# Performance work log

Hardware: AMD Instinct MI355X
Metric: run time of the kernel (lower is better)

Reference implementation:

```python
import jax, jax.numpy as jnp
import numpy as np

N = 50000

def _norm_coeffs(edge_index, n):
    # add self-loops, compute symmetric GCN normalization D^-1/2 (A+I) D^-1/2
    loops = jnp.arange(n, dtype=edge_index.dtype)
    src = jnp.concatenate([edge_index[0], loops])
    dst = jnp.concatenate([edge_index[1], loops])
    deg = jax.ops.segment_sum(jnp.ones_like(dst, dtype=jnp.float32), dst, num_segments=n)
    dinv = jnp.where(deg > 0, jax.lax.rsqrt(deg), 0.0)
    norm = dinv[src] * dinv[dst]  # [E+N]
    return src, dst, norm

def _gcn(x, W, b, src, dst, norm, n):
    h = x @ W                                   # [N, out]
    m = h[src] * norm[:, None]                  # [E+N, out] gather + scale
    return jax.ops.segment_sum(m, dst, num_segments=n) + b

def setup_inputs() -> dict:
    key = jax.random.key(0)
    ks = jax.random.split(key, 8)
    d, h = 96, 96
    E = 800000
    return {
        "x": jax.random.normal(ks[0], (N, d), jnp.float32),
        "edge_index": jax.random.randint(ks[1], (2, E), 0, N, dtype=jnp.int64),
        "h_prev": jax.random.normal(ks[2], (N, h), jnp.float32),
        "Wx": jax.random.normal(ks[3], (d, h), jnp.float32) * (1.0 / np.sqrt(d)),
        "bx": jnp.zeros((h,), jnp.float32),
        "Wuh": jax.random.normal(ks[4], (2 * h, h), jnp.float32) * (1.0 / np.sqrt(2 * h)),
        "buh": jnp.zeros((h,), jnp.float32),
        "Wch": jax.random.normal(ks[5], (2 * h, h), jnp.float32) * (1.0 / np.sqrt(2 * h)),
        "bch": jnp.zeros((h,), jnp.float32),
    }

def reference(x, edge_index, h_prev, Wx, bx, Wuh, buh, Wch, bch):
    n = x.shape[0]
    src, dst, norm = _norm_coeffs(edge_index, n)
    x_gcn = _gcn(x, Wx, bx, src, dst, norm, n)
    combined = jnp.concatenate([x_gcn, h_prev], axis=1)
    # original computes gcn_uh(combined) twice for u and r; identical math -> compute once
    g = jax.nn.sigmoid(_gcn(combined, Wuh, buh, src, dst, norm, n))
    u = g
    r = g
    combined_r = jnp.concatenate([x_gcn, r * h_prev], axis=1)
    c = jnp.tanh(_gcn(combined_r, Wch, bch, src, dst, norm, n))
    return u * h_prev + (1.0 - u) * c
```

## Files before the change

kernel.cpp:

```cpp
#include <hip/hip_runtime.h>
#include <hip/hip_bf16.h>

#define D 96
#define CAP 64
typedef long long i64;

typedef __bf16 bf16x8 __attribute__((ext_vector_type(8)));
typedef float f32x16 __attribute__((ext_vector_type(16)));

__device__ __forceinline__ float bf2f(unsigned short u) {
  union { unsigned u; float f; } x; x.u = ((unsigned)u) << 16; return x.f;
}
__device__ __forceinline__ void unpack8(uint4 p, float* a) {
  a[0] = bf2f((unsigned short)(p.x & 0xffff)); a[1] = bf2f((unsigned short)(p.x >> 16));
  a[2] = bf2f((unsigned short)(p.y & 0xffff)); a[3] = bf2f((unsigned short)(p.y >> 16));
  a[4] = bf2f((unsigned short)(p.z & 0xffff)); a[5] = bf2f((unsigned short)(p.z >> 16));
  a[6] = bf2f((unsigned short)(p.w & 0xffff)); a[7] = bf2f((unsigned short)(p.w >> 16));
}

__global__ __launch_bounds__(256) void k_detect(const unsigned* __restrict__ w,
                                                int* flag, int E) {
  if (threadIdx.x < 64) {
    int lane = threadIdx.x;
    int lim = (E < 2048) ? E : 2048;
    unsigned acc = 0;
    for (int j = lane; j < lim; j += 64) acc |= w[2 * j + 1];
#pragma unroll
    for (int off = 32; off > 0; off >>= 1) acc |= __shfl_down(acc, off, 64);
    if (lane == 0) *flag = (acc == 0) ? 1 : 0;
  }
}

__global__ __launch_bounds__(256) void k_bucket(const int* __restrict__ e32,
                                                const i64* __restrict__ e64,
                                                const int* __restrict__ flagp,
                                                uint2* __restrict__ region,
                                                int* __restrict__ cntmat,
                                                int E, int N, int NB) {
  __shared__ int lofs[256];
  const int tid = threadIdx.x;
  const int blk = blockIdx.x;
  lofs[tid] = 0;
  __syncthreads();
  const int f = *flagp;
  const int chunk = (E + gridDim.x - 1) / gridDim.x;
  const int lo = blk * chunk;
  const int hi = min(E, lo + chunk);
  for (int i = lo + tid; i < hi; i += 256) {
    int d, s;
    if (f) { d = (int)e64[(size_t)E + i]; s = (int)e64[i]; }
    else   { d = e32[(size_t)E + i];      s = e32[i]; }
    if ((unsigned)d >= (unsigned)N || (unsigned)s >= (unsigned)N) continue;
    int q = d >> 8;
    int r = atomicAdd(&lofs[q], 1);
    if (r < CAP)
      region[((size_t)q * 256 + blk) * CAP + r] = make_uint2((unsigned)s, (unsigned)d);
  }
  __syncthreads();
  if (tid < NB) cntmat[blk * 256 + tid] = min(lofs[tid], CAP);
}

__global__ __launch_bounds__(256) void k_csr(const uint2* __restrict__ region,
                                             const int* __restrict__ cntmat,
                                             int* __restrict__ deg,
                                             int* __restrict__ csrp, int NB) {
  __shared__ int ldeg[256];
  __shared__ int lcsr[256 * CAP];
  const int tid = threadIdx.x;
  const int b = blockIdx.x;
  ldeg[tid] = 0;
  __syncthreads();
  int cnt = cntmat[tid * 256 + b];
  const uint2* cell = region + ((size_t)b * 256 + tid) * CAP;
  for (int k = 0; k < cnt; k++) {
    uint2 e = cell[k];
    int node = (int)(e.y & 255u);
    int r = atomicAdd(&ldeg[node], 1);
    if (r < CAP) lcsr[node * CAP + r] = (int)e.x;
  }
  __syncthreads();
  deg[(b << 8) + tid] = ldeg[tid];
  const uint4* src = (const uint4*)lcsr;
  uint4* dst = (uint4*)(csrp + ((size_t)b << 8) * CAP);
#pragma unroll
  for (int it = 0; it < (256 * CAP) / 4 / 256; it++)
    dst[tid + it * 256] = src[tid + it * 256];
}

template <int KTOT, int MODE>
__global__ __launch_bounds__(256) void gemm_mfma(
    const float* __restrict__ xin, const float* __restrict__ xg,
    const float* __restrict__ hprev, const float* __restrict__ gmul,
    const float* __restrict__ W, const int* __restrict__ deg,
    __hip_bfloat16* __restrict__ t, int N) {
  __shared__ __align__(16) unsigned short Ah[4][129][8];
  __shared__ __align__(16) unsigned short Al[4][129][8];
  __shared__ __align__(16) unsigned short Wh[4][97][8];
  __shared__ __align__(16) unsigned short Wl[4][97][8];
  const int tid = threadIdx.x;
  const int lane = tid & 63;
  const int wave = tid >> 6;
  const int lr = lane & 31;
  const int kg = lane >> 5;
  const int rb = blockIdx.x * 128;

  f32x16 acc0, acc1, acc2;
#pragma unroll
  for (int i = 0; i < 16; i++) { acc0[i] = 0.f; acc1[i] = 0.f; acc2[i] = 0.f; }

  const int arow = tid >> 3;
  const int ak0 = (tid & 7) * 4;

  for (int kc = 0; kc < KTOT; kc += 32) {
    if (kc) __syncthreads();
#pragma unroll
    for (int p = 0; p < 4; p++) {
      int row = arow + p * 32;
      int grow = rb + row;
      float4 v = make_float4(0.f, 0.f, 0.f, 0.f);
      int gk = kc + ak0;
      if (grow < N) {
        if (MODE == 0) {
          v = *(const float4*)&xin[(size_t)grow * D + gk];
        } else if (gk < 96) {
          v = *(const float4*)&xg[(size_t)grow * D + gk];
        } else {
          v = *(const float4*)&hprev[(size_t)grow * D + (gk - 96)];
          if (MODE == 2) {
            float4 gm = *(const float4*)&gmul[(size_t)grow * D + (gk - 96)];
            v.x *= gm.x; v.y *= gm.y; v.z *= gm.z; v.w *= gm.w;
          }
        }
      }
      unsigned ux = __float_as_uint(v.x), uy = __float_as_uint(v.y);
      unsigned uz = __float_as_uint(v.z), uw = __float_as_uint(v.w);
      unsigned h01 = (uy & 0xffff0000u) | (ux >> 16);
      unsigned h23 = (uw & 0xffff0000u) | (uz >> 16);
      float lx = v.x - __uint_as_float(ux & 0xffff0000u);
      float ly = v.y - __uint_as_float(uy & 0xffff0000u);
      float lz = v.z - __uint_as_float(uz & 0xffff0000u);
      float lw = v.w - __uint_as_float(uw & 0xffff0000u);
      unsigned l01 = (__float_as_uint(ly) & 0xffff0000u) | (__float_as_uint(lx) >> 16);
      unsigned l23 = (__float_as_uint(lw) & 0xffff0000u) | (__float_as_uint(lz) >> 16);
      int kb = ak0 >> 3, ki = ak0 & 7;
      *(uint2*)&Ah[kb][row][ki] = make_uint2(h01, h23);
      *(uint2*)&Al[kb][row][ki] = make_uint2(l01, l23);
    }
#pragma unroll
    for (int p = 0; p < 3; p++) {
      int idx = tid + p * 256;
      int kq = idx / 96;
      int c = idx - kq * 96;
      int k0 = kq * 4;
      const float* wp = &W[(size_t)(kc + k0) * D + c];
      float w0 = wp[0], w1 = wp[D], w2 = wp[2 * D], w3 = wp[3 * D];
      unsigned u0 = __float_as_uint(w0), u1 = __float_as_uint(w1);
      unsigned u2 = __float_as_uint(w2), u3 = __float_as_uint(w3);
      unsigned h01 = (u1 & 0xffff0000u) | (u0 >> 16);
      unsigned h23 = (u3 & 0xffff0000u) | (u2 >> 16);
      float l0 = w0 - __uint_as_float(u0 & 0xffff0000u);
      float l1 = w1 - __uint_as_float(u1 & 0xffff0000u);
      float l2 = w2 - __uint_as_float(u2 & 0xffff0000u);
      float l3 = w3 - __uint_as_float(u3 & 0xffff0000u);
      unsigned l01 = (__float_as_uint(l1) & 0xffff0000u) | (__float_as_uint(l0) >> 16);
      unsigned l23 = (__float_as_uint(l3) & 0xffff0000u) | (__float_as_uint(l2) >> 16);
      int kb = k0 >> 3, ki = k0 & 7;
      *(uint2*)&Wh[kb][c][ki] = make_uint2(h01, h23);
      *(uint2*)&Wl[kb][c][ki] = make_uint2(l01, l23);
    }
    __syncthreads();
#pragma unroll
    for (int s = 0; s < 2; s++) {
      int kb = 2 * s + kg;
      bf16x8 ah = *(const bf16x8*)&Ah[kb][32 * wave + lr][0];
      bf16x8 al = *(const bf16x8*)&Al[kb][32 * wave + lr][0];
      bf16x8 b0h = *(const bf16x8*)&Wh[kb][lr][0];
      bf16x8 b1h = *(const bf16x8*)&Wh[kb][32 + lr][0];
      bf16x8 b2h = *(const bf16x8*)&Wh[kb][64 + lr][0];
      bf16x8 b0l = *(const bf16x8*)&Wl[kb][lr][0];
      bf16x8 b1l = *(const bf16x8*)&Wl[kb][32 + lr][0];
      bf16x8 b2l = *(const bf16x8*)&Wl[kb][64 + lr][0];
      acc0 = __builtin_amdgcn_mfma_f32_32x32x16_bf16(ah, b0h, acc0, 0, 0, 0);
      acc1 = __builtin_amdgcn_mfma_f32_32x32x16_bf16(ah, b1h, acc1, 0, 0, 0);
      acc2 = __builtin_amdgcn_mfma_f32_32x32x16_bf16(ah, b2h, acc2, 0, 0, 0);
      acc0 = __builtin_amdgcn_mfma_f32_32x32x16_bf16(al, b0h, acc0, 0, 0, 0);
      acc1 = __builtin_amdgcn_mfma_f32_32x32x16_bf16(al, b1h, acc1, 0, 0, 0);
      acc2 = __builtin_amdgcn_mfma_f32_32x32x16_bf16(al, b2h, acc2, 0, 0, 0);
      acc0 = __builtin_amdgcn_mfma_f32_32x32x16_bf16(ah, b0l, acc0, 0, 0, 0);
      acc1 = __builtin_amdgcn_mfma_f32_32x32x16_bf16(ah, b1l, acc1, 0, 0, 0);
      acc2 = __builtin_amdgcn_mfma_f32_32x32x16_bf16(ah, b2l, acc2, 0, 0, 0);
    }
  }
  const int rbase = rb + 32 * wave + 4 * kg;
#pragma unroll
  for (int r = 0; r < 16; r++) {
    int row = rbase + (r & 3) + 8 * (r >> 2);
    if (row >= N) continue;
    float dv = rsqrtf((float)deg[row] + 1.0f);
    __hip_bfloat16* tp = &t[(size_t)row * D];
    tp[lr]      = __float2bfloat16(acc0[r] * dv);
    tp[lr + 32] = __float2bfloat16(acc1[r] * dv);
    tp[lr + 64] = __float2bfloat16(acc2[r] * dv);
  }
}

template <int MODE>
__global__ __launch_bounds__(256) void gather_fin(
    const __hip_bfloat16* __restrict__ t, const int* __restrict__ deg,
    const int* __restrict__ csrp,
    const float* __restrict__ bias,
    const float* __restrict__ g, const float* __restrict__ hprev,
    float* __restrict__ outf, int N) {
  int idx = blockIdx.x * 256 + threadIdx.x;
  int total = N * 12;
  if (idx >= total) return;
  int v = idx / 12;
  int c8 = idx - v * 12;
  const uint4* t8 = (const uint4*)t;
  float acc[8];
  unpack8(t8[(size_t)v * 12 + c8], acc);
  int dv_i = deg[v];
  int b0 = v * CAP;
  int b1 = b0 + min(dv_i, CAP);
  int j = b0;
  for (; j + 8 <= b1; j += 8) {
    int s0 = csrp[j],     s1 = csrp[j + 1], s2 = csrp[j + 2], s3 = csrp[j + 3];
    int s4 = csrp[j + 4], s5 = csrp[j + 5], s6 = csrp[j + 6], s7 = csrp[j + 7];
    uint4 p0 = t8[(size_t)s0 * 12 + c8];
    uint4 p1 = t8[(size_t)s1 * 12 + c8];
    uint4 p2 = t8[(size_t)s2 * 12 + c8];
    uint4 p3 = t8[(size_t)s3 * 12 + c8];
    uint4 p4 = t8[(size_t)s4 * 12 + c8];
    uint4 p5 = t8[(size_t)s5 * 12 + c8];
    uint4 p6 = t8[(size_t)s6 * 12 + c8];
    uint4 p7 = t8[(size_t)s7 * 12 + c8];
    float a0[8], a1[8], a2[8], a3[8], a4[8], a5[8], a6[8], a7[8];
    unpack8(p0, a0); unpack8(p1, a1); unpack8(p2, a2); unpack8(p3, a3);
    unpack8(p4, a4); unpack8(p5, a5); unpack8(p6, a6); unpack8(p7, a7);
#pragma unroll
    for (int q = 0; q < 8; q++)
      acc[q] += ((a0[q] + a1[q]) + (a2[q] + a3[q])) + ((a4[q] + a5[q]) + (a6[q] + a7[q]));
  }
  for (; j + 4 <= b1; j += 4) {
    int s0 = csrp[j], s1 = csrp[j + 1], s2 = csrp[j + 2], s3 = csrp[j + 3];
    uint4 p0 = t8[(size_t)s0 * 12 + c8];
    uint4 p1 = t8[(size_t)s1 * 12 + c8];
    uint4 p2 = t8[(size_t)s2 * 12 + c8];
    uint4 p3 = t8[(size_t)s3 * 12 + c8];
    float a0[8], a1[8], a2[8], a3[8];
    unpack8(p0, a0); unpack8(p1, a1); unpack8(p2, a2); unpack8(p3, a3);
#pragma unroll
    for (int q = 0; q < 8; q++) acc[q] += (a0[q] + a1[q]) + (a2[q] + a3[q]);
  }
  for (; j < b1; j++) {
    int s = csrp[j];
    float a0[8];
    unpack8(t8[(size_t)s * 12 + c8], a0);
#pragma unroll
    for (int q = 0; q < 8; q++) acc[q] += a0[q];
  }
  float dv = rsqrtf((float)dv_i + 1.0f);
  float4 bA = ((const float4*)bias)[c8 * 2];
  float4 bB = ((const float4*)bias)[c8 * 2 + 1];
  float z[8] = {dv * acc[0] + bA.x, dv * acc[1] + bA.y, dv * acc[2] + bA.z, dv * acc[3] + bA.w,
                dv * acc[4] + bB.x, dv * acc[5] + bB.y, dv * acc[6] + bB.z, dv * acc[7] + bB.w};
  float4 oA, oB;
  if (MODE == 1) {
    oA = make_float4(z[0], z[1], z[2], z[3]);
    oB = make_float4(z[4], z[5], z[6], z[7]);
  } else if (MODE == 2) {
    oA = make_float4(1.0f / (1.0f + expf(-z[0])), 1.0f / (1.0f + expf(-z[1])),
                     1.0f / (1.0f + expf(-z[2])), 1.0f / (1.0f + expf(-z[3])));
    oB = make_float4(1.0f / (1.0f + expf(-z[4])), 1.0f / (1.0f + expf(-z[5])),
                     1.0f / (1.0f + expf(-z[6])), 1.0f / (1.0f + expf(-z[7])));
  } else {
    float4 uA = ((const float4*)g)[idx * 2], uB = ((const float4*)g)[idx * 2 + 1];
    float4 hA = ((const float4*)hprev)[idx * 2], hB = ((const float4*)hprev)[idx * 2 + 1];
    oA = make_float4(uA.x * hA.x + (1.0f - uA.x) * tanhf(z[0]),
                     uA.y * hA.y + (1.0f - uA.y) * tanhf(z[1]),
                     uA.z * hA.z + (1.0f - uA.z) * tanhf(z[2]),
                     uA.w * hA.w + (1.0f - uA.w) * tanhf(z[3]));
    oB = make_float4(uB.x * hB.x + (1.0f - uB.x) * tanhf(z[4]),
                     uB.y * hB.y + (1.0f - uB.y) * tanhf(z[5]),
                     uB.z * hB.z + (1.0f - uB.z) * tanhf(z[6]),
                     uB.w * hB.w + (1.0f - uB.w) * tanhf(z[7]));
  }
  ((float4*)outf)[idx * 2] = oA;
  ((float4*)outf)[idx * 2 + 1] = oB;
}

extern "C" void kernel_launch(void* const* d_in, const int* in_sizes, int n_in,
                              void* d_out, int out_size, void* d_ws, size_t ws_size,
                              hipStream_t stream) {
  const float* x = (const float*)d_in[0];
  const int* ei32 = (const int*)d_in[1];
  const i64* ei64 = (const i64*)d_in[1];
  const unsigned* eiw = (const unsigned*)d_in[1];
  const float* hp = (const float*)d_in[2];
  const float* Wx = (const float*)d_in[3];
  const float* bx = (const float*)d_in[4];
  const float* Wuh = (const float*)d_in[5];
  const float* buh = (const float*)d_in[6];
  const float* Wch = (const float*)d_in[7];
  const float* bch = (const float*)d_in[8];
  float* out = (float*)d_out;

  const int N = in_sizes[0] / D;
  const int E = in_sizes[1] / 2;
  const size_t NF = (size_t)N * D;
  const int NB = (N + 255) >> 8;
  const int R = NB << 8;

  char* base = (char*)d_ws;
  int* flag = (int*)base;
  int* deg = (int*)(base + 256);
  int* cntmat = deg + R;
  uint2* region = (uint2*)(cntmat + 65536);
  int* csrp = (int*)(region + (size_t)NB * 256 * CAP);
  __hip_bfloat16* t = (__hip_bfloat16*)(csrp + (size_t)R * CAP);
  float* xg = (float*)((char*)t + NF * 2);
  float* g = xg + NF;

  const int gb = (N + 127) / 128;
  const int fb8 = (N * 12 + 255) / 256;

  k_detect<<<1, 256, 0, stream>>>(eiw, flag, E);
  k_bucket<<<256, 256, 0, stream>>>(ei32, ei64, flag, region, cntmat, E, N, NB);
  k_csr<<<NB, 256, 0, stream>>>(region, cntmat, deg, csrp, NB);

  gemm_mfma<96, 0><<<gb, 256, 0, stream>>>(x, nullptr, nullptr, nullptr, Wx, deg, t, N);
  gather_fin<1><<<fb8, 256, 0, stream>>>(t, deg, csrp, bx, nullptr, nullptr, xg, N);

  gemm_mfma<192, 1><<<gb, 256, 0, stream>>>(nullptr, xg, hp, nullptr, Wuh, deg, t, N);
  gather_fin<2><<<fb8, 256, 0, stream>>>(t, deg, csrp, buh, nullptr, nullptr, g, N);

  gemm_mfma<192, 2><<<gb, 256, 0, stream>>>(nullptr, xg, hp, g, Wch, deg, t, N);
  gather_fin<3><<<fb8, 256, 0, stream>>>(t, deg, csrp, bch, g, hp, out, N);
}
```

Before: 265.8 us.

## Pre-split weights to bf16 hi/lo once and drop LDS staging in GEMM

Adds a prep kernel that converts each weight matrix once into bf16 high/low pairs laid out in MFMA operand order. The GEMM becomes a single-wave, 32-row block that loads activations straight from global memory into registers, splits them in place, and reads B fragments from the prepacked global buffers. This removes the LDS staging, the barriers and the weight conversion that every block repeated. The gather kernel also loads neighbour indices as uint4 vectors. In exchange each block now rereads the weights from cache, and the small 64-thread blocks may hide latency less well.

```diff
diff --git a/kernel.cpp b/kernel.cpp
--- a/kernel.cpp
+++ b/kernel.cpp
@@ -4,18 +4,36 @@
 #define D 96
 #define CAP 64
 typedef long long i64;
+typedef unsigned short u16;
 
 typedef __bf16 bf16x8 __attribute__((ext_vector_type(8)));
 typedef float f32x16 __attribute__((ext_vector_type(16)));
 
-__device__ __forceinline__ float bf2f(unsigned short u) {
+__device__ __forceinline__ float bf2f(u16 u) {
   union { unsigned u; float f; } x; x.u = ((unsigned)u) << 16; return x.f;
 }
 __device__ __forceinline__ void unpack8(uint4 p, float* a) {
-  a[0] = bf2f((unsigned short)(p.x & 0xffff)); a[1] = bf2f((unsigned short)(p.x >> 16));
-  a[2] = bf2f((unsigned short)(p.y & 0xffff)); a[3] = bf2f((unsigned short)(p.y >> 16));
-  a[4] = bf2f((unsigned short)(p.z & 0xffff)); a[5] = bf2f((unsigned short)(p.z >> 16));
-  a[6] = bf2f((unsigned short)(p.w & 0xffff)); a[7] = bf2f((unsigned short)(p.w >> 16));
+  a[0] = bf2f((u16)(p.x & 0xffff)); a[1] = bf2f((u16)(p.x >> 16));
+  a[2] = bf2f((u16)(p.y & 0xffff)); a[3] = bf2f((u16)(p.y >> 16));
+  a[4] = bf2f((u16)(p.z & 0xffff)); a[5] = bf2f((u16)(p.z >> 16));
+  a[6] = bf2f((u16)(p.w & 0xffff)); a[7] = bf2f((u16)(p.w >> 16));
+}
+
+__device__ __forceinline__ void split8(const float* v8, bf16x8& hi, bf16x8& lo) {
+  unsigned hu[4], lu[4];
+#pragma unroll
+  for (int p = 0; p < 4; p++) {
+    float v0 = v8[2 * p], v1 = v8[2 * p + 1];
+    unsigned u0 = __float_as_uint(v0), u1 = __float_as_uint(v1);
+    hu[p] = (u0 >> 16) | (u1 & 0xffff0000u);
+    float l0 = v0 - __uint_as_float(u0 & 0xffff0000u);
+    float l1 = v1 - __uint_as_float(u1 & 0xffff0000u);
+    lu[p] = (__float_as_uint(l0) >> 16) | (__float_as_uint(l1) & 0xffff0000u);
+  }
+  union { uint4 q; bf16x8 v; } H, L;
+  H.q = make_uint4(hu[0], hu[1], hu[2], hu[3]);
+  L.q = make_uint4(lu[0], lu[1], lu[2], lu[3]);
+  hi = H.v; lo = L.v;
 }
 
 __global__ __launch_bounds__(256) void k_detect(const unsigned* __restrict__ w,
@@ -29,6 +47,36 @@
     for (int off = 32; off > 0; off >>= 1) acc |= __shfl_down(acc, off, 64);
     if (lane == 0) *flag = (acc == 0) ? 1 : 0;
   }
+}
+
+__global__ __launch_bounds__(256) void k_wprep(const float* __restrict__ Wx,
+                                               const float* __restrict__ Wuh,
+                                               const float* __restrict__ Wch,
+                                               u16* __restrict__ wxh, u16* __restrict__ wxl,
+                                               u16* __restrict__ wuhh, u16* __restrict__ wuhl,
+                                               u16* __restrict__ wchh, u16* __restrict__ wchl) {
+  int cid = blockIdx.x * 256 + threadIdx.x;
+  const float* W; u16 *oh, *ol; int loc;
+  if (cid < 1152) { W = Wx; oh = wxh; ol = wxl; loc = cid; }
+  else if (cid < 3456) { W = Wuh; oh = wuhh; ol = wuhl; loc = cid - 1152; }
+  else if (cid < 5760) { W = Wch; oh = wchh; ol = wchl; loc = cid - 3456; }
+  else return;
+  int oct = loc / 96;
+  int j = loc - oct * 96;
+  int k0 = oct * 8;
+  unsigned hu[4], lu[4];
+#pragma unroll
+  for (int p = 0; p < 4; p++) {
+    float v0 = W[(size_t)(k0 + 2 * p) * D + j];
+    float v1 = W[(size_t)(k0 + 2 * p + 1) * D + j];
+    unsigned u0 = __float_as_uint(v0), u1 = __float_as_uint(v1);
+    hu[p] = (u0 >> 16) | (u1 & 0xffff0000u);
+    float l0 = v0 - __uint_as_float(u0 & 0xffff0000u);
+    float l1 = v1 - __uint_as_float(u1 & 0xffff0000u);
+    lu[p] = (__float_as_uint(l0) >> 16) | (__float_as_uint(l1) & 0xffff0000u);
+  }
+  *(uint4*)&oh[(size_t)loc * 8] = make_uint4(hu[0], hu[1], hu[2], hu[3]);
+  *(uint4*)&ol[(size_t)loc * 8] = make_uint4(lu[0], lu[1], lu[2], lu[3]);
 }
 
 __global__ __launch_bounds__(256) void k_bucket(const int* __restrict__ e32,
@@ -88,116 +136,77 @@
 }
 
 template <int KTOT, int MODE>
-__global__ __launch_bounds__(256) void gemm_mfma(
+__global__ __launch_bounds__(64) void gemm_mfma(
     const float* __restrict__ xin, const float* __restrict__ xg,
     const float* __restrict__ hprev, const float* __restrict__ gmul,
-    const float* __restrict__ W, const int* __restrict__ deg,
-    __hip_bfloat16* __restrict__ t, int N) {
-  __shared__ __align__(16) unsigned short Ah[4][129][8];
-  __shared__ __align__(16) unsigned short Al[4][129][8];
-  __shared__ __align__(16) unsigned short Wh[4][97][8];
-  __shared__ __align__(16) unsigned short Wl[4][97][8];
-  const int tid = threadIdx.x;
-  const int lane = tid & 63;
-  const int wave = tid >> 6;
-  const int lr = lane & 31;
-  const int kg = lane >> 5;
-  const int rb = blockIdx.x * 128;
+    const u16* __restrict__ whi, const u16* __restrict__ wlo,
+    const int* __restrict__ deg, __hip_bfloat16* __restrict__ t, int N) {
+  const int l = threadIdx.x;
+  const int lr = l & 31;
+  const int kg = l >> 5;
+  const int rb = blockIdx.x * 32;
+  const int row = rb + lr;
+  const bool rok = row < N;
 
   f32x16 acc0, acc1, acc2;
 #pragma unroll
   for (int i = 0; i < 16; i++) { acc0[i] = 0.f; acc1[i] = 0.f; acc2[i] = 0.f; }
 
-  const int arow = tid >> 3;
-  const int ak0 = (tid & 7) * 4;
-
-  for (int kc = 0; kc < KTOT; kc += 32) {
-    if (kc) __syncthreads();
-#pragma unroll
-    for (int p = 0; p < 4; p++) {
-      int row = arow + p * 32;
-      int grow = rb + row;
-      float4 v = make_float4(0.f, 0.f, 0.f, 0.f);
-      int gk = kc + ak0;
-      if (grow < N) {
-        if (MODE == 0) {
-          v = *(const float4*)&xin[(size_t)grow * D + gk];
-        } else if (gk < 96) {
-          v = *(const float4*)&xg[(size_t)grow * D + gk];
-        } else {
-          v = *(const float4*)&hprev[(size_t)grow * D + (gk - 96)];
-          if (MODE == 2) {
-            float4 gm = *(const float4*)&gmul[(size_t)grow * D + (gk - 96)];
-            v.x *= gm.x; v.y *= gm.y; v.z *= gm.z; v.w *= gm.w;
-          }
+#pragma unroll
+  for (int s = 0; s < KTOT / 16; s++) {
+    const int k0 = s * 16 + kg * 8;
+    float a8[8] = {0.f, 0.f, 0.f, 0.f, 0.f, 0.f, 0.f, 0.f};
+    if (rok) {
+      float4 va, vb;
+      if (MODE == 0) {
+        const float* src = &xin[(size_t)row * D + k0];
+        va = *(const float4*)src; vb = *(const float4*)(src + 4);
+      } else if (16 * s < 96) {
+        const float* src = &xg[(size_t)row * D + k0];
+        va = *(const float4*)src; vb = *(const float4*)(src + 4);
+      } else {
+        const float* src = &hprev[(size_t)row * D + (k0 - 96)];
+        va = *(const float4*)src; vb = *(const float4*)(src + 4);
+        if (MODE == 2) {
+          const float* gs = &gmul[(size_t)row * D + (k0 - 96)];
+          float4 ga = *(const float4*)gs, gb = *(const float4*)(gs + 4);
+          va.x *= ga.x; va.y *= ga.y; va.z *= ga.z; va.w *= ga.w;
+          vb.x *= gb.x; vb.y *= gb.y; vb.z *= gb.z; vb.w *= gb.w;
         }
       }
-      unsigned ux = __float_as_uint(v.x), uy = __float_as_uint(v.y);
-      unsigned uz = __float_as_uint(v.z), uw = __float_as_uint(v.w);
-      unsigned h01 = (uy & 0xffff0000u) | (ux >> 16);
-      unsigned h23 = (uw & 0xffff0000u) | (uz >> 16);
-      float lx = v.x - __uint_as_float(ux & 0xffff0000u);
-      float ly = v.y - __uint_as_float(uy & 0xffff0000u);
-      float lz = v.z - __uint_as_float(uz & 0xffff0000u);
-      float lw = v.w - __uint_as_float(uw & 0xffff0000u);
-      unsigned l01 = (__float_as_uint(ly) & 0xffff0000u) | (__float_as_uint(lx) >> 16);
-      unsigned l23 = (__float_as_uint(lw) & 0xffff0000u) | (__float_as_uint(lz) >> 16);
-      int kb = ak0 >> 3, ki = ak0 & 7;
-      *(uint2*)&Ah[kb][row][ki] = make_uint2(h01, h23);
-      *(uint2*)&Al[kb][row][ki] = make_uint2(l01, l23);
+      a8[0] = va.x; a8[1] = va.y; a8[2] = va.z; a8[3] = va.w;
+      a8[4] = vb.x; a8[5] = vb.y; a8[6] = vb.z; a8[7] = vb.w;
     }
-#pragma unroll
-    for (int p = 0; p < 3; p++) {
-      int idx = tid + p * 256;
-      int kq = idx / 96;
-      int c = idx - kq * 96;
-      int k0 = kq * 4;
-      const float* wp = &W[(size_t)(kc + k0) * D + c];
-      float w0 = wp[0], w1 = wp[D], w2 = wp[2 * D], w3 = wp[3 * D];
-      unsigned u0 = __float_as_uint(w0), u1 = __float_as_uint(w1);
-      unsigned u2 = __float_as_uint(w2), u3 = __float_as_uint(w3);
-      unsigned h01 = (u1 & 0xffff0000u) | (u0 >> 16);
-      unsigned h23 = (u3 & 0xffff0000u) | (u2 >> 16);
-      float l0 = w0 - __uint_as_float(u0 & 0xffff0000u);
-      float l1 = w1 - __uint_as_float(u1 & 0xffff0000u);
-      float l2 = w2 - __uint_as_float(u2 & 0xffff0000u);
-      float l3 = w3 - __uint_as_float(u3 & 0xffff0000u);
-      unsigned l01 = (__float_as_uint(l1) & 0xffff0000u) | (__float_as_uint(l0) >> 16);
-      unsigned l23 = (__float_as_uint(l3) & 0xffff0000u) | (__float_as_uint(l2) >> 16);
-      int kb = k0 >> 3, ki = k0 & 7;
-      *(uint2*)&Wh[kb][c][ki] = make_uint2(h01, h23);
-      *(uint2*)&Wl[kb][c][ki] = make_uint2(l01, l23);
-    }
-    __syncthreads();
-#pragma unroll
-    for (int s = 0; s < 2; s++) {
-      int kb = 2 * s + kg;
-      bf16x8 ah = *(const bf16x8*)&Ah[kb][32 * wave + lr][0];
-      bf16x8 al = *(const bf16x8*)&Al[kb][32 * wave + lr][0];
-      bf16x8 b0h = *(const bf16x8*)&Wh[kb][lr][0];
-      bf16x8 b1h = *(const bf16x8*)&Wh[kb][32 + lr][0];
-      bf16x8 b2h = *(const bf16x8*)&Wh[kb][64 + lr][0];
-      bf16x8 b0l = *(const bf16x8*)&Wl[kb][lr][0];
-      bf16x8 b1l = *(const bf16x8*)&Wl[kb][32 + lr][0];
-      bf16x8 b2l = *(const bf16x8*)&Wl[kb][64 + lr][0];
-      acc0 = __builtin_amdgcn_mfma_f32_32x32x16_bf16(ah, b0h, acc0, 0, 0, 0);
-      acc1 = __builtin_amdgcn_mfma_f32_32x32x16_bf16(ah, b1h, acc1, 0, 0, 0);
-      acc2 = __builtin_amdgcn_mfma_f32_32x32x16_bf16(ah, b2h, acc2, 0, 0, 0);
-      acc0 = __builtin_amdgcn_mfma_f32_32x32x16_bf16(al, b0h, acc0, 0, 0, 0);
-      acc1 = __builtin_amdgcn_mfma_f32_32x32x16_bf16(al, b1h, acc1, 0, 0, 0);
-      acc2 = __builtin_amdgcn_mfma_f32_32x32x16_bf16(al, b2h, acc2, 0, 0, 0);
-      acc0 = __builtin_amdgcn_mfma_f32_32x32x16_bf16(ah, b0l, acc0, 0, 0, 0);
-      acc1 = __builtin_amdgcn_mfma_f32_32x32x16_bf16(ah, b1l, acc1, 0, 0, 0);
-      acc2 = __builtin_amdgcn_mfma_f32_32x32x16_bf16(ah, b2l, acc2, 0, 0, 0);
-    }
-  }
-  const int rbase = rb + 32 * wave + 4 * kg;
+    bf16x8 ah, al;
+    split8(a8, ah, al);
+
+    const size_t wbase = ((size_t)(s * 2 + kg) * 96 + lr) * 8;
+    union { uint4 q; bf16x8 v; } B0h, B1h, B2h, B0l, B1l, B2l;
+    B0h.q = *(const uint4*)&whi[wbase];
+    B1h.q = *(const uint4*)&whi[wbase + 32 * 8];
+    B2h.q = *(const uint4*)&whi[wbase + 64 * 8];
+    B0l.q = *(const uint4*)&wlo[wbase];
+    B1l.q = *(const uint4*)&wlo[wbase + 32 * 8];
+    B2l.q = *(const uint4*)&wlo[wbase + 64 * 8];
+
+    acc0 = __builtin_amdgcn_mfma_f32_32x32x16_bf16(ah, B0h.v, acc0, 0, 0, 0);
+    acc1 = __builtin_amdgcn_mfma_f32_32x32x16_bf16(ah, B1h.v, acc1, 0, 0, 0);
+    acc2 = __builtin_amdgcn_mfma_f32_32x32x16_bf16(ah, B2h.v, acc2, 0, 0, 0);
+    acc0 = __builtin_amdgcn_mfma_f32_32x32x16_bf16(al, B0h.v, acc0, 0, 0, 0);
+    acc1 = __builtin_amdgcn_mfma_f32_32x32x16_bf16(al, B1h.v, acc1, 0, 0, 0);
+    acc2 = __builtin_amdgcn_mfma_f32_32x32x16_bf16(al, B2h.v, acc2, 0, 0, 0);
+    acc0 = __builtin_amdgcn_mfma_f32_32x32x16_bf16(ah, B0l.v, acc0, 0, 0, 0);
+    acc1 = __builtin_amdgcn_mfma_f32_32x32x16_bf16(ah, B1l.v, acc1, 0, 0, 0);
+    acc2 = __builtin_amdgcn_mfma_f32_32x32x16_bf16(ah, B2l.v, acc2, 0, 0, 0);
+  }
+
+  const int rbase = rb + 4 * kg;
 #pragma unroll
   for (int r = 0; r < 16; r++) {
-    int row = rbase + (r & 3) + 8 * (r >> 2);
-    if (row >= N) continue;
-    float dv = rsqrtf((float)deg[row] + 1.0f);
-    __hip_bfloat16* tp = &t[(size_t)row * D];
+    int orow = rbase + (r & 3) + 8 * (r >> 2);
+    if (orow >= N) continue;
+    float dv = rsqrtf((float)deg[orow] + 1.0f);
+    __hip_bfloat16* tp = &t[(size_t)orow * D];
     tp[lr]      = __float2bfloat16(acc0[r] * dv);
     tp[lr + 32] = __float2bfloat16(acc1[r] * dv);
     tp[lr + 64] = __float2bfloat16(acc2[r] * dv);
@@ -220,20 +229,19 @@
   float acc[8];
   unpack8(t8[(size_t)v * 12 + c8], acc);
   int dv_i = deg[v];
-  int b0 = v * CAP;
-  int b1 = b0 + min(dv_i, CAP);
-  int j = b0;
-  for (; j + 8 <= b1; j += 8) {
-    int s0 = csrp[j],     s1 = csrp[j + 1], s2 = csrp[j + 2], s3 = csrp[j + 3];
-    int s4 = csrp[j + 4], s5 = csrp[j + 5], s6 = csrp[j + 6], s7 = csrp[j + 7];
-    uint4 p0 = t8[(size_t)s0 * 12 + c8];
-    uint4 p1 = t8[(size_t)s1 * 12 + c8];
-    uint4 p2 = t8[(size_t)s2 * 12 + c8];
-    uint4 p3 = t8[(size_t)s3 * 12 + c8];
-    uint4 p4 = t8[(size_t)s4 * 12 + c8];
-    uint4 p5 = t8[(size_t)s5 * 12 + c8];
-    uint4 p6 = t8[(size_t)s6 * 12 + c8];
-    uint4 p7 = t8[(size_t)s7 * 12 + c8];
+  int nb = min(dv_i, CAP);
+  const uint4* cp = (const uint4*)(csrp + v * CAP);
+  int j = 0;
+  for (; j + 8 <= nb; j += 8) {
+    uint4 ia = cp[j >> 2], ib = cp[(j >> 2) + 1];
+    uint4 p0 = t8[(size_t)ia.x * 12 + c8];
+    uint4 p1 = t8[(size_t)ia.y * 12 + c8];
+    uint4 p2 = t8[(size_t)ia.z * 12 + c8];
+    uint4 p3 = t8[(size_t)ia.w * 12 + c8];
+    uint4 p4 = t8[(size_t)ib.x * 12 + c8];
+    uint4 p5 = t8[(size_t)ib.y * 12 + c8];
+    uint4 p6 = t8[(size_t)ib.z * 12 + c8];
+    uint4 p7 = t8[(size_t)ib.w * 12 + c8];
     float a0[8], a1[8], a2[8], a3[8], a4[8], a5[8], a6[8], a7[8];
     unpack8(p0, a0); unpack8(p1, a1); unpack8(p2, a2); unpack8(p3, a3);
     unpack8(p4, a4); unpack8(p5, a5); unpack8(p6, a6); unpack8(p7, a7);
@@ -241,19 +249,19 @@
     for (int q = 0; q < 8; q++)
       acc[q] += ((a0[q] + a1[q]) + (a2[q] + a3[q])) + ((a4[q] + a5[q]) + (a6[q] + a7[q]));
   }
-  for (; j + 4 <= b1; j += 4) {
-    int s0 = csrp[j], s1 = csrp[j + 1], s2 = csrp[j + 2], s3 = csrp[j + 3];
-    uint4 p0 = t8[(size_t)s0 * 12 + c8];
-    uint4 p1 = t8[(size_t)s1 * 12 + c8];
-    uint4 p2 = t8[(size_t)s2 * 12 + c8];
-    uint4 p3 = t8[(size_t)s3 * 12 + c8];
+  for (; j + 4 <= nb; j += 4) {
+    uint4 ia = cp[j >> 2];
+    uint4 p0 = t8[(size_t)ia.x * 12 + c8];
+    uint4 p1 = t8[(size_t)ia.y * 12 + c8];
+    uint4 p2 = t8[(size_t)ia.z * 12 + c8];
+    uint4 p3 = t8[(size_t)ia.w * 12 + c8];
     float a0[8], a1[8], a2[8], a3[8];
     unpack8(p0, a0); unpack8(p1, a1); unpack8(p2, a2); unpack8(p3, a3);
 #pragma unroll
     for (int q = 0; q < 8; q++) acc[q] += (a0[q] + a1[q]) + (a2[q] + a3[q]);
   }
-  for (; j < b1; j++) {
-    int s = csrp[j];
+  for (; j < nb; j++) {
+    int s = csrp[v * CAP + j];
     float a0[8];
     unpack8(t8[(size_t)s * 12 + c8], a0);
 #pragma unroll
@@ -313,7 +321,13 @@
 
   char* base = (char*)d_ws;
   int* flag = (int*)base;
-  int* deg = (int*)(base + 256);
+  u16* wxh = (u16*)(base + 256);
+  u16* wxl = wxh + 9216;
+  u16* wuhh = wxl + 9216;
+  u16* wuhl = wuhh + 18432;
+  u16* wchh = wuhl + 18432;
+  u16* wchl = wchh + 18432;
+  int* deg = (int*)(wchl + 18432);
   int* cntmat = deg + R;
   uint2* region = (uint2*)(cntmat + 65536);
   int* csrp = (int*)(region + (size_t)NB * 256 * CAP);
@@ -321,19 +335,20 @@
   float* xg = (float*)((char*)t + NF * 2);
   float* g = xg + NF;
 
-  const int gb = (N + 127) / 128;
+  const int gb32 = (N + 31) / 32;
   const int fb8 = (N * 12 + 255) / 256;
 
   k_detect<<<1, 256, 0, stream>>>(eiw, flag, E);
+  k_wprep<<<23, 256, 0, stream>>>(Wx, Wuh, Wch, wxh, wxl, wuhh, wuhl, wchh, wchl);
   k_bucket<<<256, 256, 0, stream>>>(ei32, ei64, flag, region, cntmat, E, N, NB);
   k_csr<<<NB, 256, 0, stream>>>(region, cntmat, deg, csrp, NB);
 
-  gemm_mfma<96, 0><<<gb, 256, 0, stream>>>(x, nullptr, nullptr, nullptr, Wx, deg, t, N);
+  gemm_mfma<96, 0><<<gb32, 64, 0, stream>>>(x, nullptr, nullptr, nullptr, wxh, wxl, deg, t, N);
   gather_fin<1><<<fb8, 256, 0, stream>>>(t, deg, csrp, bx, nullptr, nullptr, xg, N);
 
-  gemm_mfma<192, 1><<<gb, 256, 0, stream>>>(nullptr, xg, hp, nullptr, Wuh, deg, t, N);
+  gemm_mfma<192, 1><<<gb32, 64, 0, stream>>>(nullptr, xg, hp, nullptr, wuhh, wuhl, deg, t, N);
   gather_fin<2><<<fb8, 256, 0, stream>>>(t, deg, csrp, buh, nullptr, nullptr, g, N);
 
-  gemm_mfma<192, 2><<<gb, 256, 0, stream>>>(nullptr, xg, hp, g, Wch, deg, t, N);
+  gemm_mfma<192, 2><<<gb32, 64, 0, stream>>>(nullptr, xg, hp, g, wchh, wchl, deg, t, N);
   gather_fin<3><<<fb8, 256, 0, stream>>>(t, deg, csrp, bch, g, hp, out, N);
 }
```

Result: no change. 261.0 us (-1.8%).
